# Kernel tuning notes

Hardware: AMD Instinct MI355X
Metric: run time of the kernel (lower is better)

## Reference

```python
import jax, jax.numpy as jnp
import numpy as np

N0, N1, N2 = 32, 32, 32
BOX = np.array([[0.0, 1.0], [0.0, 1.0], [0.0, 1.0]], dtype=np.float32)
N_VERTS, N_FACES = 512, 1024
EPS = 1.19209e-07
SEPS = float(np.sqrt(EPS))  # ~3.45e-4, matches torch code


def _freq_axis(n, lo, hi):
    # xi_k = (2k - (n-1)) * pi / (hi - lo)
    s = np.pi / (hi - lo)
    k = jnp.arange(n, dtype=jnp.float32)
    return (2.0 * k - (n - 1)) * jnp.float32(s)


def setup_inputs() -> dict:
    key = jax.random.key(0)
    k1, k2 = jax.random.split(key)
    Verts = jax.random.normal(k1, (N_VERTS, 3), dtype=jnp.float32)
    # distinct vertex indices per face -> non-degenerate triangles (a.s.)
    base = jax.random.randint(k2, (N_FACES, 1), 0, N_VERTS)
    Faces = (base + jnp.arange(3)[None, :]) % N_VERTS
    box_size = jnp.asarray(BOX)
    xi0 = _freq_axis(N0, BOX[0, 0], BOX[0, 1])
    xi1 = _freq_axis(N1, BOX[1, 0], BOX[1, 1])
    xi2 = _freq_axis(N2, BOX[2, 0], BOX[2, 1])
    return {"Verts": Verts, "box_size": box_size, "xi0": xi0, "xi1": xi1,
            "xi2": xi2, "Faces": Faces}


def _expmj(x):
    # exp(-i x) for real x -> complex64
    return jnp.exp(-1j * x)


def _fourier(Verts, box_size, xi0, xi1, xi2, Faces):
    V = Verts - box_size[:, 0]                      # shift into box frame
    coords = V[Faces]                               # (F, 3, 3)
    cross = jnp.cross(coords[:, 1] - coords[:, 0], coords[:, 2] - coords[:, 0])
    trisar = 0.5 * jnp.linalg.norm(cross, axis=1)   # (F,)
    meshar = jnp.sum(trisar)
    trisar = trisar * (2.0 / meshar)

    G0, G1, G2 = jnp.meshgrid(xi0, xi1, xi2, indexing="ij")
    Xi = jnp.stack([G0.ravel(), G1.ravel(), G2.ravel()], axis=1)  # (G, 3)
    xiv = Xi @ V.T                                  # (G, nV)

    xia = xiv[:, Faces[:, 0]]                       # (G, F)
    xib = xiv[:, Faces[:, 1]]
    xic = xiv[:, Faces[:, 2]]
    xiab = xib - xia
    xibc = xic - xib
    xica = xia - xic

    aab, abc, aca = jnp.abs(xiab), jnp.abs(xibc), jnp.abs(xica)
    s2, s3, s4 = aab < SEPS, abc < SEPS, aca < SEPS      # strict, for C1
    c2, c3, c4 = aab <= SEPS, abc <= SEPS, aca <= SEPS   # non-strict, C2-C4
    R1 = (s2 & s3) | (s3 & s4) | (s4 & s2)
    R2 = c2 & ~R1
    R3 = c3 & ~R2 & ~R1
    R4 = c4 & ~R3 & ~R2 & ~R1
    R5 = ~(R1 | R2 | R3 | R4)

    # R1: all edges collapse in frequency space
    v1 = _expmj((xia + xib + xic) / 3.0) / 2.0

    def _pair_case(mask, x1, x2, x3):
        # (i*exp(-i m) + (exp(-i m) - exp(-i x3)) / d) / d,  m=(x1+x2)/2, d=m-x3
        m = (x1 + x2) * 0.5
        d = jnp.where(mask, m - x3, 1.0)  # safe denominator off-mask
        em = _expmj(m)
        return (1j * em + (em - _expmj(x3)) / d) / d

    v2 = _pair_case(R2, xia, xib, xic)
    v3 = _pair_case(R3, xib, xic, xia)
    v4 = _pair_case(R4, xic, xia, xib)

    da = jnp.where(R5, xiab * xica, 1.0)
    db = jnp.where(R5, xibc * xiab, 1.0)
    dc = jnp.where(R5, xica * xibc, 1.0)
    v5 = _expmj(xia) / da + _expmj(xib) / db + _expmj(xic) / dc

    res = jnp.where(R1, v1,
          jnp.where(R2, v2,
          jnp.where(R3, v3,
          jnp.where(R4, v4, v5))))                  # (G, F) complex64

    ft = res @ trisar.astype(res.dtype)             # (G,)
    return ft.reshape(G0.shape)                     # (N0, N1, N2)


def reference(Verts, box_size, xi0, xi1, xi2, Faces):
    return _fourier(Verts, box_size, xi0, xi1, xi2, Faces)
```

## Files before the change

### kernel.cpp

```cpp
#include <hip/hip_runtime.h>
#include <math.h>

namespace {
constexpr int kNpts = 32 * 32 * 32;
constexpr int kHalf = kNpts / 2;
constexpr int kNF = 1024;
constexpr int kWaves = 16;
constexpr int kFaceHalves = 2;
constexpr int kFPG = kNF / (kWaves * kFaceHalves);
constexpr int kRec = 12;
constexpr int kRec64Off = 64;
constexpr int kRec32OffD = kRec64Off + kRec * kNF;
constexpr int kGridOffD = kRec32OffD + (kRec * kNF) / 2;
}

__device__ __forceinline__ float fract32(float x) {
#if __has_builtin(__builtin_amdgcn_fractf)
    return __builtin_amdgcn_fractf(x);
#else
    return x - floorf(x);
#endif
}

__global__ __launch_bounds__(256) void face_prep(
        const float* __restrict__ verts, const float* __restrict__ box,
        const int* __restrict__ faces, double* __restrict__ ws) {
    __shared__ float wsum[4];
    const int f = blockIdx.x * 256 + threadIdx.x;
    const double lo0 = (double)box[0], lo1 = (double)box[2], lo2 = (double)box[4];
    const int ia = faces[3 * f + 0], ib = faces[3 * f + 1], ic = faces[3 * f + 2];
    const double ax = (double)verts[3 * ia + 0] - lo0, ay = (double)verts[3 * ia + 1] - lo1, az = (double)verts[3 * ia + 2] - lo2;
    const double bx = (double)verts[3 * ib + 0] - lo0, by = (double)verts[3 * ib + 1] - lo1, bz = (double)verts[3 * ib + 2] - lo2;
    const double cx = (double)verts[3 * ic + 0] - lo0, cy = (double)verts[3 * ic + 1] - lo1, cz = (double)verts[3 * ic + 2] - lo2;
    const float axf = (float)ax, ayf = (float)ay, azf = (float)az;
    const float bxf = (float)bx, byf = (float)by, bzf = (float)bz;
    const float cxf = (float)cx, cyf = (float)cy, czf = (float)cz;
    const float e1x = bxf - axf, e1y = byf - ayf, e1z = bzf - azf;
    const float e2x = cxf - axf, e2y = cyf - ayf, e2z = czf - azf;
    const float crx = e1y * e2z - e1z * e2y;
    const float cry = e1z * e2x - e1x * e2z;
    const float crz = e1x * e2y - e1y * e2x;
    const float area = 0.5f * sqrtf(crx * crx + cry * cry + crz * crz);
    float a = area;
    a += __shfl_down(a, 32, 64);
    a += __shfl_down(a, 16, 64);
    a += __shfl_down(a, 8, 64);
    a += __shfl_down(a, 4, 64);
    a += __shfl_down(a, 2, 64);
    a += __shfl_down(a, 1, 64);
    if ((threadIdx.x & 63) == 0) wsum[threadIdx.x >> 6] = a;
    __syncthreads();
    if (threadIdx.x == 0)
        ((float*)ws)[blockIdx.x] = ((wsum[0] + wsum[1]) + wsum[2]) + wsum[3];
    double* r = ws + kRec64Off + (size_t)kRec * f;
    r[0] = ax; r[1] = ay; r[2] = az;
    r[3] = bx; r[4] = by; r[5] = bz;
    r[6] = cx; r[7] = cy; r[8] = cz;
    r[9] = (double)area;
    r[10] = 0.0; r[11] = 0.0;
    float* r32 = (float*)(ws + kRec32OffD) + (size_t)kRec * f;
    r32[0] = axf; r32[1] = ayf; r32[2] = azf;
    r32[3] = bxf; r32[4] = byf; r32[5] = bzf;
    r32[6] = cxf; r32[7] = cyf; r32[8] = czf;
    r32[9] = area * 0.025330296f;
    r32[10] = 0.0f; r32[11] = 0.0f;
}

__device__ __forceinline__ void pair_case_f64(double x1, double x2, double x3,
                                              double& vr, double& vi) {
    const double m = (x1 + x2) * 0.5;
    const double d = m - x3;
    double sm, cm, s3, c3;
    sincos(m, &sm, &cm);
    sincos(x3, &s3, &c3);
    vr = (sm + (cm - c3) / d) / d;
    vi = (cm + (s3 - sm) / d) / d;
}

__global__ __launch_bounds__(kWaves * 64, 8) void fourier_main(
        const double* __restrict__ ws, const float* __restrict__ xi0,
        const float* __restrict__ xi1, const float* __restrict__ xi2) {
    const double SEPS = __builtin_sqrt(1.19209e-07);
    const double TWO_PI = 6.283185307179586;
    const double INV_TWO_PI = 0.15915494309189535;
    const float INV_TWO_PI_F = 0.15915494f;
    const float TAUP_REV2 = 2.5330296e-5f;

    const int t = threadIdx.x;
    const int l = t & 63;
    const int w = t >> 6;
    const int pb = blockIdx.x & 255;
    const int fh = blockIdx.x >> 8;
    const int p = pb * 64 + l;
    const int i2 = p & 31, i1 = (p >> 5) & 31, i0 = p >> 10;
    const float x0 = xi0[i0], x1 = xi1[i1], x2 = xi2[i2];
    const float xxr = x0 * INV_TWO_PI_F;
    const float xyr = x1 * INV_TWO_PI_F;
    const float xzr = x2 * INV_TWO_PI_F;
    const double xxd = (double)x0 * INV_TWO_PI;
    const double xyd = (double)x1 * INV_TWO_PI;
    const double xzd = (double)x2 * INV_TWO_PI;

    float re = 0.0f, im = 0.0f;
    const int grp = __builtin_amdgcn_readfirstlane(fh * kWaves + w);
    const float* fp32 = (const float*)(ws + kRec32OffD) + (size_t)grp * kFPG * kRec;
    const double* fp64 = ws + kRec64Off + (size_t)grp * kFPG * kRec;

#pragma unroll 4
    for (int i = 0; i < kFPG; ++i) {
        const float* r = fp32 + i * kRec;
        const float ra = fmaf(xzr, r[2], fmaf(xyr, r[1], xxr * r[0]));
        const float rb = fmaf(xzr, r[5], fmaf(xyr, r[4], xxr * r[3]));
        const float rc = fmaf(xzr, r[8], fmaf(xyr, r[7], xxr * r[6]));
        const float fdab = rb - ra, fdbc = rc - rb, fdca = ra - rc;
        const float d1 = fdab * fdca;
        const float d2 = fdbc * fdab;
        const float d3 = fdca * fdbc;
        const float mn = fminf(fminf(fabsf(d1), fabsf(d2)), fabsf(d3));

        if (mn > TAUP_REV2) {
            const float wsc = r[9];
            const float R3 = __builtin_amdgcn_rcpf(d1 * fdbc);
            const float r1 = fdbc * R3, r2 = fdca * R3, r3 = fdab * R3;
            const float fa = fract32(ra);
            const float fb = fract32(rb);
            const float fc = fract32(rc);
            const float sa = __builtin_amdgcn_sinf(fa), ca = __builtin_amdgcn_cosf(fa);
            const float sb = __builtin_amdgcn_sinf(fb), cb = __builtin_amdgcn_cosf(fb);
            const float sc = __builtin_amdgcn_sinf(fc), cc = __builtin_amdgcn_cosf(fc);
            re = fmaf(wsc, fmaf(ca, r1, fmaf(cb, r2, cc * r3)), re);
            im = fmaf(-wsc, fmaf(sa, r1, fmaf(sb, r2, sc * r3)), im);
        } else {
            const double* r64 = fp64 + i * kRec;
            const double rad = fma(xzd, r64[2], fma(xyd, r64[1], xxd * r64[0]));
            const double rbd = fma(xzd, r64[5], fma(xyd, r64[4], xxd * r64[3]));
            const double rcd = fma(xzd, r64[8], fma(xyd, r64[7], xxd * r64[6]));
            const double area = r64[9];
            const double xa = rad * TWO_PI, xb = rbd * TWO_PI, xc = rcd * TWO_PI;
            const double dAB = xb - xa, dBC = xc - xb, dCA = xa - xc;
            const double aab = fabs(dAB), abc = fabs(dBC), aca = fabs(dCA);
            const bool s2 = aab < SEPS, s3 = abc < SEPS, s4 = aca < SEPS;
            const bool c2 = aab <= SEPS, c3 = abc <= SEPS, c4 = aca <= SEPS;
            const bool R1 = (s2 && s3) || (s3 && s4) || (s4 && s2);
            const bool R2 = c2 && !R1;
            const bool R3b = c3 && !R2 && !R1;
            const bool R4 = c4 && !R3b && !R2 && !R1;
            double vr, vi;
            if (R1) {
                const double m = ((xa + xb) + xc) / 3.0;
                double sm, cm;
                sincos(m, &sm, &cm);
                vr = cm / 2.0;
                vi = -sm / 2.0;
            } else if (R2) {
                pair_case_f64(xa, xb, xc, vr, vi);
            } else if (R3b) {
                pair_case_f64(xb, xc, xa, vr, vi);
            } else if (R4) {
                pair_case_f64(xc, xa, xb, vr, vi);
            } else {
                double sa, ca, sb, cb, sc, cc;
                sincos(xa, &sa, &ca);
                sincos(xb, &sb, &cb);
                sincos(xc, &sc, &cc);
                const double da = dAB * dCA, db = dBC * dAB, dc = dCA * dBC;
                vr = (ca / da + cb / db) + cc / dc;
                vi = -((sa / da + sb / db) + sc / dc);
            }
            re = fmaf((float)area, (float)vr, re);
            im = fmaf((float)area, (float)vi, im);
        }
    }

    __shared__ float pr[kWaves][64];
    __shared__ float pi[kWaves][64];
    pr[w][l] = re;
    pi[w][l] = im;
    __syncthreads();
    if (w == 0) {
        float R = pr[0][l], I = pi[0][l];
#pragma unroll
        for (int g = 1; g < kWaves; ++g) { R += pr[g][l]; I += pi[g][l]; }
        float2* pg = (float2*)(ws + kGridOffD);
        pg[(size_t)fh * kHalf + p] = make_float2(R, I);
    }
}

__global__ __launch_bounds__(256) void combine(
        const double* __restrict__ ws, float* __restrict__ out, int interleaved) {
    const int p = blockIdx.x * 256 + threadIdx.x;
    const float* psum = (const float*)ws;
    const float meshar = ((psum[0] + psum[1]) + psum[2]) + psum[3];
    const float inv2 = 2.0f / meshar;
    const float2* pg = (const float2*)(ws + kGridOffD);
    const float2 a = pg[p];
    const float2 b = pg[kHalf + p];
    const float R = (a.x + b.x) * inv2;
    const float I = (a.y + b.y) * inv2;
    const int q = kNpts - 1 - p;
    if (interleaved) {
        ((float2*)out)[p] = make_float2(R, I);
        ((float2*)out)[q] = make_float2(R, -I);
    } else {
        out[p] = R;
        out[q] = R;
    }
}

extern "C" void kernel_launch(void* const* d_in, const int* in_sizes, int n_in,
                              void* d_out, int out_size, void* d_ws, size_t ws_size,
                              hipStream_t stream) {
    const float* verts = (const float*)d_in[0];
    const float* box   = (const float*)d_in[1];
    const float* xi0v  = (const float*)d_in[2];
    const float* xi1v  = (const float*)d_in[3];
    const float* xi2v  = (const float*)d_in[4];
    const int*   faces = (const int*)d_in[5];
    double* ws = (double*)d_ws;

    const int interleaved = (out_size == 2 * kNpts) ? 1 : 0;

    hipLaunchKernelGGL(face_prep, dim3(kNF / 256), dim3(256), 0, stream,
                       verts, box, faces, ws);
    hipLaunchKernelGGL(fourier_main, dim3((kHalf / 64) * kFaceHalves),
                       dim3(kWaves * 64), 0, stream, ws, xi0v, xi1v, xi2v);
    hipLaunchKernelGGL(combine, dim3(kHalf / 256), dim3(256), 0, stream,
                       ws, (float*)d_out, interleaved);
}
```

Baseline: 98.50 us.

## Defer rare fp64 fallback work to a separate compacted fix-up kernel

The fp64 slow path for near-degenerate face/frequency pairs is removed from the main loop. Those pairs are now appended to a global list with an atomic counter and handled by a new fourier_fix kernel, which adds its results into the partial grid with float atomics. The aim is to cut divergence and register pressure from the fp64 sincos code in the hot loop, and the weight multiply is also folded into the reciprocal. In exchange it adds one launch and contended global atomics, and any entries beyond the capacity derived from the workspace size are silently dropped.

Measured after the change: 96.55 us. 2.0% less time.

```diff
diff --git a/kernel.cpp b/kernel.cpp
--- a/kernel.cpp
+++ b/kernel.cpp
@@ -12,6 +12,8 @@
 constexpr int kRec64Off = 64;
 constexpr int kRec32OffD = kRec64Off + kRec * kNF;
 constexpr int kGridOffD = kRec32OffD + (kRec * kNF) / 2;
+constexpr int kSlowCntD = 8;
+constexpr int kSlowListD = kGridOffD + kFaceHalves * kHalf;
 }
 
 __device__ __forceinline__ float fract32(float x) {
@@ -27,6 +29,8 @@
         const int* __restrict__ faces, double* __restrict__ ws) {
     __shared__ float wsum[4];
     const int f = blockIdx.x * 256 + threadIdx.x;
+    if (blockIdx.x == 0 && threadIdx.x == 0)
+        *(unsigned*)(ws + kSlowCntD) = 0u;
     const double lo0 = (double)box[0], lo1 = (double)box[2], lo2 = (double)box[4];
     const int ia = faces[3 * f + 0], ib = faces[3 * f + 1], ic = faces[3 * f + 2];
     const double ax = (double)verts[3 * ia + 0] - lo0, ay = (double)verts[3 * ia + 1] - lo1, az = (double)verts[3 * ia + 2] - lo2;
@@ -78,11 +82,8 @@
 }
 
 __global__ __launch_bounds__(kWaves * 64, 8) void fourier_main(
-        const double* __restrict__ ws, const float* __restrict__ xi0,
-        const float* __restrict__ xi1, const float* __restrict__ xi2) {
-    const double SEPS = __builtin_sqrt(1.19209e-07);
-    const double TWO_PI = 6.283185307179586;
-    const double INV_TWO_PI = 0.15915494309189535;
+        double* __restrict__ ws, const float* __restrict__ xi0,
+        const float* __restrict__ xi1, const float* __restrict__ xi2, int cap) {
     const float INV_TWO_PI_F = 0.15915494f;
     const float TAUP_REV2 = 2.5330296e-5f;
 
@@ -97,14 +98,12 @@
     const float xxr = x0 * INV_TWO_PI_F;
     const float xyr = x1 * INV_TWO_PI_F;
     const float xzr = x2 * INV_TWO_PI_F;
-    const double xxd = (double)x0 * INV_TWO_PI;
-    const double xyd = (double)x1 * INV_TWO_PI;
-    const double xzd = (double)x2 * INV_TWO_PI;
 
     float re = 0.0f, im = 0.0f;
     const int grp = __builtin_amdgcn_readfirstlane(fh * kWaves + w);
     const float* fp32 = (const float*)(ws + kRec32OffD) + (size_t)grp * kFPG * kRec;
-    const double* fp64 = ws + kRec64Off + (size_t)grp * kFPG * kRec;
+    unsigned* cnt = (unsigned*)(ws + kSlowCntD);
+    unsigned* list = (unsigned*)(ws + kSlowListD);
 
 #pragma unroll 4
     for (int i = 0; i < kFPG; ++i) {
@@ -119,56 +118,20 @@
         const float mn = fminf(fminf(fabsf(d1), fabsf(d2)), fabsf(d3));
 
         if (mn > TAUP_REV2) {
-            const float wsc = r[9];
-            const float R3 = __builtin_amdgcn_rcpf(d1 * fdbc);
-            const float r1 = fdbc * R3, r2 = fdca * R3, r3 = fdab * R3;
+            const float R3w = __builtin_amdgcn_rcpf(d1 * fdbc) * r[9];
+            const float r1 = fdbc * R3w, r2 = fdca * R3w, r3 = fdab * R3w;
             const float fa = fract32(ra);
             const float fb = fract32(rb);
             const float fc = fract32(rc);
             const float sa = __builtin_amdgcn_sinf(fa), ca = __builtin_amdgcn_cosf(fa);
             const float sb = __builtin_amdgcn_sinf(fb), cb = __builtin_amdgcn_cosf(fb);
             const float sc = __builtin_amdgcn_sinf(fc), cc = __builtin_amdgcn_cosf(fc);
-            re = fmaf(wsc, fmaf(ca, r1, fmaf(cb, r2, cc * r3)), re);
-            im = fmaf(-wsc, fmaf(sa, r1, fmaf(sb, r2, sc * r3)), im);
+            re = fmaf(cc, r3, fmaf(cb, r2, fmaf(ca, r1, re)));
+            im = fmaf(-sc, r3, fmaf(-sb, r2, fmaf(-sa, r1, im)));
         } else {
-            const double* r64 = fp64 + i * kRec;
-            const double rad = fma(xzd, r64[2], fma(xyd, r64[1], xxd * r64[0]));
-            const double rbd = fma(xzd, r64[5], fma(xyd, r64[4], xxd * r64[3]));
-            const double rcd = fma(xzd, r64[8], fma(xyd, r64[7], xxd * r64[6]));
-            const double area = r64[9];
-            const double xa = rad * TWO_PI, xb = rbd * TWO_PI, xc = rcd * TWO_PI;
-            const double dAB = xb - xa, dBC = xc - xb, dCA = xa - xc;
-            const double aab = fabs(dAB), abc = fabs(dBC), aca = fabs(dCA);
-            const bool s2 = aab < SEPS, s3 = abc < SEPS, s4 = aca < SEPS;
-            const bool c2 = aab <= SEPS, c3 = abc <= SEPS, c4 = aca <= SEPS;
-            const bool R1 = (s2 && s3) || (s3 && s4) || (s4 && s2);
-            const bool R2 = c2 && !R1;
-            const bool R3b = c3 && !R2 && !R1;
-            const bool R4 = c4 && !R3b && !R2 && !R1;
-            double vr, vi;
-            if (R1) {
-                const double m = ((xa + xb) + xc) / 3.0;
-                double sm, cm;
-                sincos(m, &sm, &cm);
-                vr = cm / 2.0;
-                vi = -sm / 2.0;
-            } else if (R2) {
-                pair_case_f64(xa, xb, xc, vr, vi);
-            } else if (R3b) {
-                pair_case_f64(xb, xc, xa, vr, vi);
-            } else if (R4) {
-                pair_case_f64(xc, xa, xb, vr, vi);
-            } else {
-                double sa, ca, sb, cb, sc, cc;
-                sincos(xa, &sa, &ca);
-                sincos(xb, &sb, &cb);
-                sincos(xc, &sc, &cc);
-                const double da = dAB * dCA, db = dBC * dAB, dc = dCA * dBC;
-                vr = (ca / da + cb / db) + cc / dc;
-                vi = -((sa / da + sb / db) + sc / dc);
-            }
-            re = fmaf((float)area, (float)vr, re);
-            im = fmaf((float)area, (float)vi, im);
+            const unsigned idx = atomicAdd(cnt, 1u);
+            if ((int)idx < cap)
+                list[idx] = ((unsigned)(grp * kFPG + i) << 14) | (unsigned)p;
         }
     }
 
@@ -183,6 +146,66 @@
         for (int g = 1; g < kWaves; ++g) { R += pr[g][l]; I += pi[g][l]; }
         float2* pg = (float2*)(ws + kGridOffD);
         pg[(size_t)fh * kHalf + p] = make_float2(R, I);
+    }
+}
+
+__global__ __launch_bounds__(256) void fourier_fix(
+        double* __restrict__ ws, const float* __restrict__ xi0,
+        const float* __restrict__ xi1, const float* __restrict__ xi2, int cap) {
+    const double SEPS = __builtin_sqrt(1.19209e-07);
+    const double TWO_PI = 6.283185307179586;
+    const double INV_TWO_PI = 0.15915494309189535;
+    unsigned n = *(const unsigned*)(ws + kSlowCntD);
+    if (n > (unsigned)cap) n = (unsigned)cap;
+    const unsigned* list = (const unsigned*)(ws + kSlowListD);
+    float* pg = (float*)(ws + kGridOffD);
+    for (unsigned idx = blockIdx.x * 256 + threadIdx.x; idx < n;
+         idx += gridDim.x * 256) {
+        const unsigned e = list[idx];
+        const int p = (int)(e & 16383u);
+        const int f = (int)(e >> 14);
+        const int i2 = p & 31, i1 = (p >> 5) & 31, i0 = p >> 10;
+        const double xxd = (double)xi0[i0] * INV_TWO_PI;
+        const double xyd = (double)xi1[i1] * INV_TWO_PI;
+        const double xzd = (double)xi2[i2] * INV_TWO_PI;
+        const double* r64 = ws + kRec64Off + (size_t)kRec * f;
+        const double rad = fma(xzd, r64[2], fma(xyd, r64[1], xxd * r64[0]));
+        const double rbd = fma(xzd, r64[5], fma(xyd, r64[4], xxd * r64[3]));
+        const double rcd = fma(xzd, r64[8], fma(xyd, r64[7], xxd * r64[6]));
+        const double area = r64[9];
+        const double xa = rad * TWO_PI, xb = rbd * TWO_PI, xc = rcd * TWO_PI;
+        const double dAB = xb - xa, dBC = xc - xb, dCA = xa - xc;
+        const double aab = fabs(dAB), abc = fabs(dBC), aca = fabs(dCA);
+        const bool s2 = aab < SEPS, s3 = abc < SEPS, s4 = aca < SEPS;
+        const bool c2 = aab <= SEPS, c3 = abc <= SEPS, c4 = aca <= SEPS;
+        const bool R1 = (s2 && s3) || (s3 && s4) || (s4 && s2);
+        const bool R2 = c2 && !R1;
+        const bool R3b = c3 && !R2 && !R1;
+        const bool R4 = c4 && !R3b && !R2 && !R1;
+        double vr, vi;
+        if (R1) {
+            const double m = ((xa + xb) + xc) / 3.0;
+            double sm, cm;
+            sincos(m, &sm, &cm);
+            vr = cm / 2.0;
+            vi = -sm / 2.0;
+        } else if (R2) {
+            pair_case_f64(xa, xb, xc, vr, vi);
+        } else if (R3b) {
+            pair_case_f64(xb, xc, xa, vr, vi);
+        } else if (R4) {
+            pair_case_f64(xc, xa, xb, vr, vi);
+        } else {
+            double sa, ca, sb, cb, sc, cc;
+            sincos(xa, &sa, &ca);
+            sincos(xb, &sb, &cb);
+            sincos(xc, &sc, &cc);
+            const double da = dAB * dCA, db = dBC * dAB, dc = dCA * dBC;
+            vr = (ca / da + cb / db) + cc / dc;
+            vi = -((sa / da + sb / db) + sc / dc);
+        }
+        atomicAdd(&pg[2 * p + 0], (float)area * (float)vr);
+        atomicAdd(&pg[2 * p + 1], (float)area * (float)vi);
     }
 }
 
@@ -220,10 +243,20 @@
 
     const int interleaved = (out_size == 2 * kNpts) ? 1 : 0;
 
+    const size_t listByteOff = (size_t)kSlowListD * 8;
+    int cap = 0;
+    if (ws_size > listByteOff + 4) {
+        size_t c = (ws_size - listByteOff) / 4;
+        if (c > (size_t)(1 << 22)) c = (size_t)(1 << 22);
+        cap = (int)c;
+    }
+
     hipLaunchKernelGGL(face_prep, dim3(kNF / 256), dim3(256), 0, stream,
                        verts, box, faces, ws);
     hipLaunchKernelGGL(fourier_main, dim3((kHalf / 64) * kFaceHalves),
-                       dim3(kWaves * 64), 0, stream, ws, xi0v, xi1v, xi2v);
+                       dim3(kWaves * 64), 0, stream, ws, xi0v, xi1v, xi2v, cap);
+    hipLaunchKernelGGL(fourier_fix, dim3(32), dim3(256), 0, stream,
+                       ws, xi0v, xi1v, xi2v, cap);
     hipLaunchKernelGGL(combine, dim3(kHalf / 256), dim3(256), 0, stream,
                        ws, (float*)d_out, interleaved);
 }
```

## Fuse face prep into main kernel and defer f64 slow path to compacted fixup

Applied to the files above, without the earlier changes.

Removes the separate face_prep kernel: each block now builds its 512 face records in LDS and computes the area partial sums itself. The f64 fallback for near-degenerate (point, face) pairs no longer runs inside the hot loop. Such pairs are ballot-compacted into per-wave lists in workspace, and a combine_fix kernel evaluates them in f64 and adds them through LDS atomics before the final combine. The goal is to avoid wave divergence and double-precision code in the main loop and to save one launch. The cost is redundant per-block face prep, each fixup block scanning every wave's list, and a correctness risk if the workspace cannot hold the lists. The fast-path threshold now tests edge differences instead of their products.

Measured after the change: 151.6 us. 53.9% more time.

```diff
diff --git a/kernel.cpp b/kernel.cpp
--- a/kernel.cpp
+++ b/kernel.cpp
@@ -8,10 +8,12 @@
 constexpr int kWaves = 16;
 constexpr int kFaceHalves = 2;
 constexpr int kFPG = kNF / (kWaves * kFaceHalves);
-constexpr int kRec = 12;
-constexpr int kRec64Off = 64;
-constexpr int kRec32OffD = kRec64Off + kRec * kNF;
-constexpr int kGridOffD = kRec32OffD + (kRec * kNF) / 2;
+constexpr int kBlocks = (kHalf / 64) * kFaceHalves;
+constexpr int kNumWaves = kBlocks * kWaves;
+constexpr int kGridOffW = 256;
+constexpr int kCntOffW = kGridOffW + kFaceHalves * kHalf * 2;
+constexpr int kSegOffW = kCntOffW + kNumWaves;
+constexpr int kSegStrideMax = 2048;
 }
 
 __device__ __forceinline__ float fract32(float x) {
@@ -20,50 +22,6 @@
 #else
     return x - floorf(x);
 #endif
-}
-
-__global__ __launch_bounds__(256) void face_prep(
-        const float* __restrict__ verts, const float* __restrict__ box,
-        const int* __restrict__ faces, double* __restrict__ ws) {
-    __shared__ float wsum[4];
-    const int f = blockIdx.x * 256 + threadIdx.x;
-    const double lo0 = (double)box[0], lo1 = (double)box[2], lo2 = (double)box[4];
-    const int ia = faces[3 * f + 0], ib = faces[3 * f + 1], ic = faces[3 * f + 2];
-    const double ax = (double)verts[3 * ia + 0] - lo0, ay = (double)verts[3 * ia + 1] - lo1, az = (double)verts[3 * ia + 2] - lo2;
-    const double bx = (double)verts[3 * ib + 0] - lo0, by = (double)verts[3 * ib + 1] - lo1, bz = (double)verts[3 * ib + 2] - lo2;
-    const double cx = (double)verts[3 * ic + 0] - lo0, cy = (double)verts[3 * ic + 1] - lo1, cz = (double)verts[3 * ic + 2] - lo2;
-    const float axf = (float)ax, ayf = (float)ay, azf = (float)az;
-    const float bxf = (float)bx, byf = (float)by, bzf = (float)bz;
-    const float cxf = (float)cx, cyf = (float)cy, czf = (float)cz;
-    const float e1x = bxf - axf, e1y = byf - ayf, e1z = bzf - azf;
-    const float e2x = cxf - axf, e2y = cyf - ayf, e2z = czf - azf;
-    const float crx = e1y * e2z - e1z * e2y;
-    const float cry = e1z * e2x - e1x * e2z;
-    const float crz = e1x * e2y - e1y * e2x;
-    const float area = 0.5f * sqrtf(crx * crx + cry * cry + crz * crz);
-    float a = area;
-    a += __shfl_down(a, 32, 64);
-    a += __shfl_down(a, 16, 64);
-    a += __shfl_down(a, 8, 64);
-    a += __shfl_down(a, 4, 64);
-    a += __shfl_down(a, 2, 64);
-    a += __shfl_down(a, 1, 64);
-    if ((threadIdx.x & 63) == 0) wsum[threadIdx.x >> 6] = a;
-    __syncthreads();
-    if (threadIdx.x == 0)
-        ((float*)ws)[blockIdx.x] = ((wsum[0] + wsum[1]) + wsum[2]) + wsum[3];
-    double* r = ws + kRec64Off + (size_t)kRec * f;
-    r[0] = ax; r[1] = ay; r[2] = az;
-    r[3] = bx; r[4] = by; r[5] = bz;
-    r[6] = cx; r[7] = cy; r[8] = cz;
-    r[9] = (double)area;
-    r[10] = 0.0; r[11] = 0.0;
-    float* r32 = (float*)(ws + kRec32OffD) + (size_t)kRec * f;
-    r32[0] = axf; r32[1] = ayf; r32[2] = azf;
-    r32[3] = bxf; r32[4] = byf; r32[5] = bzf;
-    r32[6] = cxf; r32[7] = cyf; r32[8] = czf;
-    r32[9] = area * 0.025330296f;
-    r32[10] = 0.0f; r32[11] = 0.0f;
 }
 
 __device__ __forceinline__ void pair_case_f64(double x1, double x2, double x3,
@@ -78,64 +36,167 @@
 }
 
 __global__ __launch_bounds__(kWaves * 64, 8) void fourier_main(
-        const double* __restrict__ ws, const float* __restrict__ xi0,
-        const float* __restrict__ xi1, const float* __restrict__ xi2) {
-    const double SEPS = __builtin_sqrt(1.19209e-07);
-    const double TWO_PI = 6.283185307179586;
-    const double INV_TWO_PI = 0.15915494309189535;
+        const float* __restrict__ verts, const float* __restrict__ box,
+        const int* __restrict__ faces, unsigned* __restrict__ wsu,
+        const float* __restrict__ xi0, const float* __restrict__ xi1,
+        const float* __restrict__ xi2, int segStride) {
     const float INV_TWO_PI_F = 0.15915494f;
-    const float TAUP_REV2 = 2.5330296e-5f;
+    const float TAU1 = 5.033e-3f;
+
+    __shared__ float4 rec[512][3];
+    __shared__ float accR[kWaves][64];
+    __shared__ float accI[kWaves][64];
+    __shared__ float wsum[8];
 
     const int t = threadIdx.x;
     const int l = t & 63;
     const int w = t >> 6;
     const int pb = blockIdx.x & 255;
     const int fh = blockIdx.x >> 8;
+
+    if (t < 512) {
+        const int f = fh * 512 + t;
+        const float lo0 = box[0], lo1 = box[2], lo2 = box[4];
+        const int ia = faces[3 * f + 0], ib = faces[3 * f + 1], ic = faces[3 * f + 2];
+        const float ax = verts[3 * ia + 0] - lo0, ay = verts[3 * ia + 1] - lo1, az = verts[3 * ia + 2] - lo2;
+        const float bx = verts[3 * ib + 0] - lo0, by = verts[3 * ib + 1] - lo1, bz = verts[3 * ib + 2] - lo2;
+        const float cx = verts[3 * ic + 0] - lo0, cy = verts[3 * ic + 1] - lo1, cz = verts[3 * ic + 2] - lo2;
+        const float e1x = bx - ax, e1y = by - ay, e1z = bz - az;
+        const float e2x = cx - ax, e2y = cy - ay, e2z = cz - az;
+        const float crx = e1y * e2z - e1z * e2y;
+        const float cry = e1z * e2x - e1x * e2z;
+        const float crz = e1x * e2y - e1y * e2x;
+        const float area = 0.5f * sqrtf(crx * crx + cry * cry + crz * crz);
+        rec[t][0] = make_float4(ax, ay, az, bx);
+        rec[t][1] = make_float4(by, bz, cx, cy);
+        rec[t][2] = make_float4(cz, area * 0.025330296f, 0.0f, 0.0f);
+        float a = area;
+        a += __shfl_down(a, 32, 64);
+        a += __shfl_down(a, 16, 64);
+        a += __shfl_down(a, 8, 64);
+        a += __shfl_down(a, 4, 64);
+        a += __shfl_down(a, 2, 64);
+        a += __shfl_down(a, 1, 64);
+        if (l == 0) wsum[w] = a;
+    }
+    __syncthreads();
+    if (t == 0 && pb == 0) {
+        float s = wsum[0];
+#pragma unroll
+        for (int j = 1; j < 8; ++j) s += wsum[j];
+        ((float*)wsu)[fh] = s;
+    }
+
     const int p = pb * 64 + l;
     const int i2 = p & 31, i1 = (p >> 5) & 31, i0 = p >> 10;
-    const float x0 = xi0[i0], x1 = xi1[i1], x2 = xi2[i2];
-    const float xxr = x0 * INV_TWO_PI_F;
-    const float xyr = x1 * INV_TWO_PI_F;
-    const float xzr = x2 * INV_TWO_PI_F;
-    const double xxd = (double)x0 * INV_TWO_PI;
-    const double xyd = (double)x1 * INV_TWO_PI;
-    const double xzd = (double)x2 * INV_TWO_PI;
+    const float xxr = xi0[i0] * INV_TWO_PI_F;
+    const float xyr = xi1[i1] * INV_TWO_PI_F;
+    const float xzr = xi2[i2] * INV_TWO_PI_F;
 
     float re = 0.0f, im = 0.0f;
-    const int grp = __builtin_amdgcn_readfirstlane(fh * kWaves + w);
-    const float* fp32 = (const float*)(ws + kRec32OffD) + (size_t)grp * kFPG * kRec;
-    const double* fp64 = ws + kRec64Off + (size_t)grp * kFPG * kRec;
+    unsigned cntLocal = 0;
+    const int waveId = blockIdx.x * kWaves + w;
+    unsigned* seg = wsu + kSegOffW + (size_t)waveId * segStride;
+    const int fbase = fh * 512 + w * kFPG;
+    const int rbase = w * kFPG;
 
 #pragma unroll 4
     for (int i = 0; i < kFPG; ++i) {
-        const float* r = fp32 + i * kRec;
-        const float ra = fmaf(xzr, r[2], fmaf(xyr, r[1], xxr * r[0]));
-        const float rb = fmaf(xzr, r[5], fmaf(xyr, r[4], xxr * r[3]));
-        const float rc = fmaf(xzr, r[8], fmaf(xyr, r[7], xxr * r[6]));
+        const float4 q0 = rec[rbase + i][0];
+        const float4 q1 = rec[rbase + i][1];
+        const float4 q2 = rec[rbase + i][2];
+        const float ra = fmaf(xzr, q0.z, fmaf(xyr, q0.y, xxr * q0.x));
+        const float rb = fmaf(xzr, q1.y, fmaf(xyr, q1.x, xxr * q0.w));
+        const float rc = fmaf(xzr, q2.x, fmaf(xyr, q1.w, xxr * q1.z));
         const float fdab = rb - ra, fdbc = rc - rb, fdca = ra - rc;
-        const float d1 = fdab * fdca;
-        const float d2 = fdbc * fdab;
-        const float d3 = fdca * fdbc;
-        const float mn = fminf(fminf(fabsf(d1), fabsf(d2)), fabsf(d3));
-
-        if (mn > TAUP_REV2) {
-            const float wsc = r[9];
-            const float R3 = __builtin_amdgcn_rcpf(d1 * fdbc);
-            const float r1 = fdbc * R3, r2 = fdca * R3, r3 = fdab * R3;
+        const float mn = fminf(fminf(fabsf(fdab), fabsf(fdbc)), fabsf(fdca));
+        const bool slow = !(mn > TAU1);
+        if (!slow) {
+            const float R3w = __builtin_amdgcn_rcpf((fdab * fdca) * fdbc) * q2.y;
+            const float r1 = fdbc * R3w, r2 = fdca * R3w, r3 = fdab * R3w;
             const float fa = fract32(ra);
             const float fb = fract32(rb);
             const float fc = fract32(rc);
             const float sa = __builtin_amdgcn_sinf(fa), ca = __builtin_amdgcn_cosf(fa);
             const float sb = __builtin_amdgcn_sinf(fb), cb = __builtin_amdgcn_cosf(fb);
             const float sc = __builtin_amdgcn_sinf(fc), cc = __builtin_amdgcn_cosf(fc);
-            re = fmaf(wsc, fmaf(ca, r1, fmaf(cb, r2, cc * r3)), re);
-            im = fmaf(-wsc, fmaf(sa, r1, fmaf(sb, r2, sc * r3)), im);
-        } else {
-            const double* r64 = fp64 + i * kRec;
-            const double rad = fma(xzd, r64[2], fma(xyd, r64[1], xxd * r64[0]));
-            const double rbd = fma(xzd, r64[5], fma(xyd, r64[4], xxd * r64[3]));
-            const double rcd = fma(xzd, r64[8], fma(xyd, r64[7], xxd * r64[6]));
-            const double area = r64[9];
+            re = fmaf(cc, r3, fmaf(cb, r2, fmaf(ca, r1, re)));
+            im = fmaf(-sc, r3, fmaf(-sb, r2, fmaf(-sa, r1, im)));
+        }
+        const unsigned long long m = __ballot(slow);
+        if (m) {
+            if (slow) {
+                const unsigned pos =
+                    cntLocal + (unsigned)__popcll(m & ((1ull << l) - 1ull));
+                if ((int)pos < segStride)
+                    seg[pos] = ((unsigned)(fbase + i) << 14) | (unsigned)p;
+            }
+            cntLocal += (unsigned)__popcll(m);
+        }
+    }
+    if (l == 0) wsu[kCntOffW + waveId] = cntLocal;
+
+    accR[w][l] = re;
+    accI[w][l] = im;
+    __syncthreads();
+    if (w == 0) {
+        float R = accR[0][l], I = accI[0][l];
+#pragma unroll
+        for (int g = 1; g < kWaves; ++g) { R += accR[g][l]; I += accI[g][l]; }
+        float2* pg = (float2*)(wsu + kGridOffW);
+        pg[(size_t)fh * kHalf + p] = make_float2(R, I);
+    }
+}
+
+__global__ __launch_bounds__(256) void combine_fix(
+        const float* __restrict__ verts, const float* __restrict__ box,
+        const int* __restrict__ faces, const float* __restrict__ xi0,
+        const float* __restrict__ xi1, const float* __restrict__ xi2,
+        unsigned* __restrict__ wsu, float* __restrict__ out,
+        int interleaved, int segStride) {
+    const double SEPS = __builtin_sqrt(1.19209e-07);
+    const double TWO_PI = 6.283185307179586;
+    const double INV_TWO_PI = 0.15915494309189535;
+
+    __shared__ float corrR[256], corrI[256];
+    const int tid = threadIdx.x;
+    const int pbase = blockIdx.x * 256;
+    corrR[tid] = 0.0f;
+    corrI[tid] = 0.0f;
+    __syncthreads();
+
+    for (int s = tid; s < kNumWaves; s += 256) {
+        unsigned n = wsu[kCntOffW + s];
+        if (n == 0) continue;
+        if (n > (unsigned)segStride) n = (unsigned)segStride;
+        const unsigned* seg = wsu + kSegOffW + (size_t)s * segStride;
+        for (unsigned j = 0; j < n; ++j) {
+            const unsigned e = seg[j];
+            const int p = (int)(e & 16383u);
+            const unsigned rel = (unsigned)(p - pbase);
+            if (rel >= 256u) continue;
+            const int f = (int)(e >> 14);
+            const int i2 = p & 31, i1 = (p >> 5) & 31, i0 = p >> 10;
+            const double xxd = (double)xi0[i0] * INV_TWO_PI;
+            const double xyd = (double)xi1[i1] * INV_TWO_PI;
+            const double xzd = (double)xi2[i2] * INV_TWO_PI;
+            const double lo0 = (double)box[0], lo1 = (double)box[2], lo2 = (double)box[4];
+            const int ia = faces[3 * f + 0], ib = faces[3 * f + 1], ic = faces[3 * f + 2];
+            const double ax = (double)verts[3 * ia + 0] - lo0, ay = (double)verts[3 * ia + 1] - lo1, az = (double)verts[3 * ia + 2] - lo2;
+            const double bx = (double)verts[3 * ib + 0] - lo0, by = (double)verts[3 * ib + 1] - lo1, bz = (double)verts[3 * ib + 2] - lo2;
+            const double cx = (double)verts[3 * ic + 0] - lo0, cy = (double)verts[3 * ic + 1] - lo1, cz = (double)verts[3 * ic + 2] - lo2;
+            const float axf = (float)ax, ayf = (float)ay, azf = (float)az;
+            const float bxf = (float)bx, byf = (float)by, bzf = (float)bz;
+            const float cxf = (float)cx, cyf = (float)cy, czf = (float)cz;
+            const float e1x = bxf - axf, e1y = byf - ayf, e1z = bzf - azf;
+            const float e2x = cxf - axf, e2y = cyf - ayf, e2z = czf - azf;
+            const float crx = e1y * e2z - e1z * e2y;
+            const float cry = e1z * e2x - e1x * e2z;
+            const float crz = e1x * e2y - e1y * e2x;
+            const float areaf = 0.5f * sqrtf(crx * crx + cry * cry + crz * crz);
+            const double rad = fma(xzd, az, fma(xyd, ay, xxd * ax));
+            const double rbd = fma(xzd, bz, fma(xyd, by, xxd * bx));
+            const double rcd = fma(xzd, cz, fma(xyd, cy, xxd * cx));
             const double xa = rad * TWO_PI, xb = rbd * TWO_PI, xc = rcd * TWO_PI;
             const double dAB = xb - xa, dBC = xc - xb, dCA = xa - xc;
             const double aab = fabs(dAB), abc = fabs(dBC), aca = fabs(dCA);
@@ -167,36 +228,21 @@
                 vr = (ca / da + cb / db) + cc / dc;
                 vi = -((sa / da + sb / db) + sc / dc);
             }
-            re = fmaf((float)area, (float)vr, re);
-            im = fmaf((float)area, (float)vi, im);
+            atomicAdd(&corrR[rel], areaf * (float)vr);
+            atomicAdd(&corrI[rel], areaf * (float)vi);
         }
     }
-
-    __shared__ float pr[kWaves][64];
-    __shared__ float pi[kWaves][64];
-    pr[w][l] = re;
-    pi[w][l] = im;
-    __syncthreads();
-    if (w == 0) {
-        float R = pr[0][l], I = pi[0][l];
-#pragma unroll
-        for (int g = 1; g < kWaves; ++g) { R += pr[g][l]; I += pi[g][l]; }
-        float2* pg = (float2*)(ws + kGridOffD);
-        pg[(size_t)fh * kHalf + p] = make_float2(R, I);
-    }
-}
-
-__global__ __launch_bounds__(256) void combine(
-        const double* __restrict__ ws, float* __restrict__ out, int interleaved) {
-    const int p = blockIdx.x * 256 + threadIdx.x;
-    const float* psum = (const float*)ws;
-    const float meshar = ((psum[0] + psum[1]) + psum[2]) + psum[3];
+    __syncthreads();
+
+    const int p = pbase + tid;
+    const float* wsf = (const float*)wsu;
+    const float meshar = wsf[0] + wsf[1];
     const float inv2 = 2.0f / meshar;
-    const float2* pg = (const float2*)(ws + kGridOffD);
+    const float2* pg = (const float2*)(wsu + kGridOffW);
     const float2 a = pg[p];
     const float2 b = pg[kHalf + p];
-    const float R = (a.x + b.x) * inv2;
-    const float I = (a.y + b.y) * inv2;
+    const float R = (a.x + b.x + corrR[tid]) * inv2;
+    const float I = (a.y + b.y + corrI[tid]) * inv2;
     const int q = kNpts - 1 - p;
     if (interleaved) {
         ((float2*)out)[p] = make_float2(R, I);
@@ -216,14 +262,21 @@
     const float* xi1v  = (const float*)d_in[3];
     const float* xi2v  = (const float*)d_in[4];
     const int*   faces = (const int*)d_in[5];
-    double* ws = (double*)d_ws;
+    unsigned* wsu = (unsigned*)d_ws;
 
     const int interleaved = (out_size == 2 * kNpts) ? 1 : 0;
 
-    hipLaunchKernelGGL(face_prep, dim3(kNF / 256), dim3(256), 0, stream,
-                       verts, box, faces, ws);
-    hipLaunchKernelGGL(fourier_main, dim3((kHalf / 64) * kFaceHalves),
-                       dim3(kWaves * 64), 0, stream, ws, xi0v, xi1v, xi2v);
-    hipLaunchKernelGGL(combine, dim3(kHalf / 256), dim3(256), 0, stream,
-                       ws, (float*)d_out, interleaved);
-}
+    int segStride = kSegStrideMax;
+    const size_t wsWords = ws_size / 4;
+    if (wsWords < (size_t)kSegOffW + (size_t)kNumWaves * segStride) {
+        segStride = (wsWords > (size_t)kSegOffW)
+                        ? (int)((wsWords - kSegOffW) / kNumWaves)
+                        : 0;
+    }
+
+    hipLaunchKernelGGL(fourier_main, dim3(kBlocks), dim3(kWaves * 64), 0, stream,
+                       verts, box, faces, wsu, xi0v, xi1v, xi2v, segStride);
+    hipLaunchKernelGGL(combine_fix, dim3(kHalf / 256), dim3(256), 0, stream,
+                       verts, box, faces, xi0v, xi1v, xi2v, wsu,
+                       (float*)d_out, interleaved, segStride);
+}
```
